# Optimization experiments

Hardware: AMD Instinct MI355X
Metric: run time of the kernel (lower is better)

## Reference

```python
import jax, jax.numpy as jnp
import numpy as np

N_POINTS = 16384  # matches init_kwargs n_points


def setup_inputs() -> dict:
    key = jax.random.key(0)
    k1, k2 = jax.random.split(key)
    B, N = 32, 524288
    p = jax.random.normal(k1, (B, N, 3), dtype=jnp.float32)
    zero_mask = jax.random.bernoulli(k2, 0.3, (B, N))
    p = jnp.where(zero_mask[..., None], 0.0, p)
    return {"pred_cloud": p}


def _sample_one(key, p):
    # p: (N, 3). Torch: non_zeros = sum(p, dim=2).ne(0); filter, then
    # randperm[:n] if enough points else randint with replacement.
    N = p.shape[0]
    mask = jnp.sum(p, axis=1) != 0              # (N,) valid points
    k = jnp.sum(mask).astype(jnp.int32)          # number of valid points
    # stable argsort puts valid (False for ~mask) indices first -> compacted index list
    order = jnp.argsort(~mask, stable=True)      # (N,)
    kperm, krep = jax.random.split(key)
    # branch A (k >= n_points): random subset without replacement among valid
    scores = jnp.where(mask, jax.random.uniform(kperm, (N,)), jnp.inf)
    perm_idx = jnp.argsort(scores)[:N_POINTS]    # (n_points,) valid indices, random order
    # branch B (k < n_points): randint(0, k) with replacement over compacted valid ids
    u = jax.random.uniform(krep, (N_POINTS,))
    rep = jnp.floor(u * k.astype(u.dtype)).astype(jnp.int32) % jnp.maximum(k, 1)
    repl_idx = order[rep]
    idx = jnp.where(k < N_POINTS, repl_idx, perm_idx)  # (n_points,)
    return p[idx]                                 # (n_points, 3)


def reference(pred_cloud):
    B = pred_cloud.shape[0]
    keys = jax.random.split(jax.random.key(42), B)
    return jax.vmap(_sample_one)(keys, pred_cloud)  # (B, n_points, 3)
```

## Files before the change

### kernel.cpp

```cpp
#include <hip/hip_runtime.h>
#include <stdint.h>

#define NB 32
#define NN 524288
#define NPTS 16384
#define NSEG 8
#define SEGCAP 4096
#define SCAP 20480
#define NBINS 4096
#define THRESH 0.0478515625f
#define CNTSTRIDE 32

struct Keys { uint32_t k[2 * NB]; };

__host__ __device__ static inline void tf2x32(uint32_t k0, uint32_t k1,
                                              uint32_t x0, uint32_t x1,
                                              uint32_t* o0, uint32_t* o1) {
  uint32_t ks2 = k0 ^ k1 ^ 0x1BD11BDAu;
  x0 += k0; x1 += k1;
#define TFR(r) { x0 += x1; x1 = (x1 << (r)) | (x1 >> (32 - (r))); x1 ^= x0; }
  TFR(13) TFR(15) TFR(26) TFR(6)
  x0 += k1; x1 += ks2 + 1u;
  TFR(17) TFR(29) TFR(16) TFR(24)
  x0 += ks2; x1 += k0 + 2u;
  TFR(13) TFR(15) TFR(26) TFR(6)
  x0 += k0; x1 += k1 + 3u;
  TFR(17) TFR(29) TFR(16) TFR(24)
  x0 += k1; x1 += ks2 + 4u;
  TFR(13) TFR(15) TFR(26) TFR(6)
  x0 += ks2; x1 += k0 + 5u;
#undef TFR
  *o0 = x0; *o1 = x1;
}

__global__ __launch_bounds__(256) void k_candidates(
    const float* __restrict__ p, Keys keys,
    uint64_t* __restrict__ cand, uint32_t* __restrict__ cand_cnt) {
  const int b = blockIdx.y;
  const int t = threadIdx.x;
  const int i0 = (blockIdx.x * 256 + t) * 4;
  const uint32_t kp0 = keys.k[2 * b], kp1 = keys.k[2 * b + 1];
  const float* pb = p + (size_t)b * NN * 3;

  uint64_t mykeys[4];
  int nc = 0;
#pragma unroll
  for (int j = 0; j < 4; ++j) {
    uint32_t o0, o1;
    tf2x32(kp0, kp1, 0u, (uint32_t)(i0 + j), &o0, &o1);
    uint32_t bits = o0 ^ o1;
    float u = __uint_as_float((bits >> 9) | 0x3F800000u) - 1.0f;
    if (u < THRESH) {
      const float* pp = pb + 3 * (size_t)(i0 + j);
      float x = pp[0], y = pp[1], z = pp[2];
      if (((x + y) + z) != 0.0f)
        mykeys[nc++] = ((uint64_t)__float_as_uint(u) << 32) | (uint32_t)(i0 + j);
    }
  }

  __shared__ uint32_t lcnt, lbase;
  if (t == 0) lcnt = 0u;
  __syncthreads();
  uint32_t loc = 0u;
  if (nc) loc = atomicAdd(&lcnt, (uint32_t)nc);
  __syncthreads();
  const int seg = blockIdx.x & (NSEG - 1);
  if (t == 0)
    lbase = atomicAdd(&cand_cnt[(b * NSEG + seg) * CNTSTRIDE], lcnt);
  __syncthreads();
  uint64_t* cb = cand + ((size_t)b * NSEG + seg) * SEGCAP;
  for (int j = 0; j < nc; ++j) {
    uint32_t slot = lbase + loc + j;
    if (slot < SEGCAP) cb[slot] = mykeys[j];
  }
}

__global__ __launch_bounds__(1024) void k_scan_scatter(
    const uint64_t* __restrict__ cand, const uint32_t* __restrict__ cand_cnt,
    uint32_t* __restrict__ cum, uint32_t* __restrict__ scount,
    uint64_t* __restrict__ sorted) {
  const int b = blockIdx.x;
  const int t = threadIdx.x;
  const int lane = t & 63, wave = t >> 6;
  __shared__ uint32_t lhist[NBINS];
  __shared__ uint32_t lcum[NBINS + 1];
  __shared__ uint32_t wsum[16];
  __shared__ uint32_t segM[NSEG];

  for (int i = t; i < NBINS; i += 1024) lhist[i] = 0u;
  if (t < NSEG) {
    uint32_t M = cand_cnt[(b * NSEG + t) * CNTSTRIDE];
    segM[t] = (M > SEGCAP) ? SEGCAP : M;
  }
  __syncthreads();

#pragma unroll
  for (int s = 0; s < NSEG; ++s) {
    const uint32_t M = segM[s];
    const uint64_t* cb = cand + ((size_t)b * NSEG + s) * SEGCAP;
    for (uint32_t j = t; j < M; j += 1024) {
      uint32_t ub = (uint32_t)(cb[j] >> 32);
      int bin = (int)(__uint_as_float(ub) * 65536.0f);
      atomicAdd(&lhist[bin], 1u);
    }
  }
  __syncthreads();

  uint32_t h0 = lhist[4 * t], h1 = lhist[4 * t + 1],
           h2 = lhist[4 * t + 2], h3 = lhist[4 * t + 3];
  uint32_t s4 = h0 + h1 + h2 + h3;
  uint32_t v = s4;
  for (int off = 1; off < 64; off <<= 1) {
    uint32_t n = __shfl_up(v, off, 64);
    if (lane >= off) v += n;
  }
  if (lane == 63) wsum[wave] = v;
  __syncthreads();
  if (t < 16) {
    uint32_t w = wsum[t];
    for (int off = 1; off < 16; off <<= 1) {
      uint32_t n = __shfl_up(w, off, 64);
      if (t >= off) w += n;
    }
    wsum[t] = w;
  }
  __syncthreads();
  uint32_t incl = v + (wave ? wsum[wave - 1] : 0u);
  uint32_t c[5];
  c[0] = incl - s4; c[1] = c[0] + h0; c[2] = c[1] + h1;
  c[3] = c[2] + h2; c[4] = incl;
  lcum[4 * t] = c[0]; lcum[4 * t + 1] = c[1];
  lcum[4 * t + 2] = c[2]; lcum[4 * t + 3] = c[3];
  if (t == 1023) lcum[NBINS] = incl;
  uint32_t* gc = cum + (size_t)b * (NBINS + 1);
  gc[4 * t] = c[0]; gc[4 * t + 1] = c[1];
  gc[4 * t + 2] = c[2]; gc[4 * t + 3] = c[3];
  if (t == 1023) gc[NBINS] = incl;
#pragma unroll
  for (int q = 0; q < 4; ++q)
    if (c[q] < NPTS && c[q + 1] >= NPTS) {
      uint32_t sc = c[q + 1];
      scount[b] = (sc > SCAP) ? SCAP : sc;
    }
  if (t == 1023 && incl < NPTS) scount[b] = incl;
  __syncthreads();

  for (int i = t; i < NBINS; i += 1024) lhist[i] = 0u;
  __syncthreads();
#pragma unroll
  for (int s = 0; s < NSEG; ++s) {
    const uint32_t M = segM[s];
    const uint64_t* cb = cand + ((size_t)b * NSEG + s) * SEGCAP;
    for (uint32_t j = t; j < M; j += 1024) {
      uint64_t key = cb[j];
      int bin = (int)(__uint_as_float((uint32_t)(key >> 32)) * 65536.0f);
      uint32_t c0 = lcum[bin];
      if (c0 < NPTS) {
        uint32_t pos = atomicAdd(&lhist[bin], 1u);
        uint32_t sl = c0 + pos;
        if (sl < SCAP) sorted[(size_t)b * SCAP + sl] = key;
      }
    }
  }
}

__global__ __launch_bounds__(256) void k_rank(
    const float* __restrict__ p, const uint64_t* __restrict__ sorted,
    const uint32_t* __restrict__ cum, const uint32_t* __restrict__ scount,
    float* __restrict__ out) {
  const int b = blockIdx.y;
  const uint32_t j = blockIdx.x * 256 + threadIdx.x;
  if (j >= scount[b]) return;
  const uint64_t* sb = sorted + (size_t)b * SCAP;
  uint64_t key = sb[j];
  float u = __uint_as_float((uint32_t)(key >> 32));
  int bin = (int)(u * 65536.0f);
  const uint32_t* gc = cum + (size_t)b * (NBINS + 1);
  uint32_t c0 = gc[bin], c1 = gc[bin + 1];
  uint32_t r = c0;
  for (uint32_t l = c0; l < c1; ++l) r += (sb[l] < key) ? 1u : 0u;
  if (r < NPTS) {
    uint32_t idx = (uint32_t)key;
    const float* pp = p + (size_t)b * NN * 3 + 3 * (size_t)idx;
    float* o = out + ((size_t)b * NPTS + r) * 3;
    o[0] = pp[0]; o[1] = pp[1]; o[2] = pp[2];
  }
}

extern "C" void kernel_launch(void* const* d_in, const int* in_sizes, int n_in,
                              void* d_out, int out_size, void* d_ws, size_t ws_size,
                              hipStream_t stream) {
  const float* p = (const float*)d_in[0];
  float* out = (float*)d_out;
  uint8_t* ws = (uint8_t*)d_ws;

  size_t off_cand   = 0;
  size_t off_sorted = off_cand + (size_t)NB * NSEG * SEGCAP * 8;
  size_t off_cum    = off_sorted + (size_t)NB * SCAP * 8;
  size_t off_scnt   = off_cum + (size_t)NB * (NBINS + 1) * 4;
  size_t off_cnt    = off_scnt + 128;
  size_t zero_bytes = (size_t)NB * NSEG * CNTSTRIDE * 4;

  uint64_t* cand     = (uint64_t*)(ws + off_cand);
  uint64_t* sorted   = (uint64_t*)(ws + off_sorted);
  uint32_t* cum      = (uint32_t*)(ws + off_cum);
  uint32_t* scount   = (uint32_t*)(ws + off_scnt);
  uint32_t* cand_cnt = (uint32_t*)(ws + off_cnt);

  Keys keys;
  for (int b = 0; b < NB; ++b) {
    uint32_t kb0, kb1, kp0, kp1;
    tf2x32(0u, 42u, 0u, (uint32_t)b, &kb0, &kb1);
    tf2x32(kb0, kb1, 0u, 0u, &kp0, &kp1);
    keys.k[2 * b] = kp0; keys.k[2 * b + 1] = kp1;
  }

  hipMemsetAsync(ws + off_cnt, 0, zero_bytes, stream);
  dim3 g1(NN / 1024, NB);
  k_candidates<<<g1, 256, 0, stream>>>(p, keys, cand, cand_cnt);
  k_scan_scatter<<<NB, 1024, 0, stream>>>(cand, cand_cnt, cum, scount, sorted);
  dim3 g4(SCAP / 256, NB);
  k_rank<<<g4, 256, 0, stream>>>(p, sorted, cum, scount, out);
}
```

Measured before the change: 308.5 us.

## Store candidates in fixed per-block slots instead of global atomic segments

Each candidate block now writes its filtered keys into a private fixed-capacity slot (BCAP entries) and records its count. This removes the global atomic append counters and the memset that zeroed them. The scan kernel maps two threads to each producer block's slot and reads per-block counts. A 2-float vector load for the point xy and removal of one barrier are also included. Any block producing more than BCAP candidates silently drops the excess. BCAP is sized for the roughly 49 expected candidates per block.

```diff
diff --git a/kernel.cpp b/kernel.cpp
--- a/kernel.cpp
+++ b/kernel.cpp
@@ -4,12 +4,11 @@
 #define NB 32
 #define NN 524288
 #define NPTS 16384
-#define NSEG 8
-#define SEGCAP 4096
+#define NBLK (NN / 1024)
+#define BCAP 96
 #define SCAP 20480
 #define NBINS 4096
 #define THRESH 0.0478515625f
-#define CNTSTRIDE 32
 
 struct Keys { uint32_t k[2 * NB]; };
 
@@ -35,12 +34,14 @@
 
 __global__ __launch_bounds__(256) void k_candidates(
     const float* __restrict__ p, Keys keys,
-    uint64_t* __restrict__ cand, uint32_t* __restrict__ cand_cnt) {
+    uint64_t* __restrict__ cand, uint32_t* __restrict__ blkcnt) {
   const int b = blockIdx.y;
+  const int bx = blockIdx.x;
   const int t = threadIdx.x;
-  const int i0 = (blockIdx.x * 256 + t) * 4;
+  const int i0 = (bx * 256 + t) * 4;
   const uint32_t kp0 = keys.k[2 * b], kp1 = keys.k[2 * b + 1];
   const float* pb = p + (size_t)b * NN * 3;
+  typedef float f2 __attribute__((ext_vector_type(2), aligned(4)));
 
   uint64_t mykeys[4];
   int nc = 0;
@@ -52,31 +53,29 @@
     float u = __uint_as_float((bits >> 9) | 0x3F800000u) - 1.0f;
     if (u < THRESH) {
       const float* pp = pb + 3 * (size_t)(i0 + j);
-      float x = pp[0], y = pp[1], z = pp[2];
-      if (((x + y) + z) != 0.0f)
+      f2 v = *(const f2*)pp;
+      float z = pp[2];
+      if (((v.x + v.y) + z) != 0.0f)
         mykeys[nc++] = ((uint64_t)__float_as_uint(u) << 32) | (uint32_t)(i0 + j);
     }
   }
 
-  __shared__ uint32_t lcnt, lbase;
+  __shared__ uint32_t lcnt;
   if (t == 0) lcnt = 0u;
   __syncthreads();
   uint32_t loc = 0u;
   if (nc) loc = atomicAdd(&lcnt, (uint32_t)nc);
   __syncthreads();
-  const int seg = blockIdx.x & (NSEG - 1);
-  if (t == 0)
-    lbase = atomicAdd(&cand_cnt[(b * NSEG + seg) * CNTSTRIDE], lcnt);
-  __syncthreads();
-  uint64_t* cb = cand + ((size_t)b * NSEG + seg) * SEGCAP;
+  uint64_t* cb = cand + ((size_t)b * NBLK + bx) * BCAP;
   for (int j = 0; j < nc; ++j) {
-    uint32_t slot = lbase + loc + j;
-    if (slot < SEGCAP) cb[slot] = mykeys[j];
-  }
+    uint32_t sl = loc + j;
+    if (sl < BCAP) cb[sl] = mykeys[j];
+  }
+  if (t == 0) blkcnt[b * NBLK + bx] = (lcnt > BCAP) ? BCAP : lcnt;
 }
 
 __global__ __launch_bounds__(1024) void k_scan_scatter(
-    const uint64_t* __restrict__ cand, const uint32_t* __restrict__ cand_cnt,
+    const uint64_t* __restrict__ cand, const uint32_t* __restrict__ blkcnt,
     uint32_t* __restrict__ cum, uint32_t* __restrict__ scount,
     uint64_t* __restrict__ sorted) {
   const int b = blockIdx.x;
@@ -85,23 +84,22 @@
   __shared__ uint32_t lhist[NBINS];
   __shared__ uint32_t lcum[NBINS + 1];
   __shared__ uint32_t wsum[16];
-  __shared__ uint32_t segM[NSEG];
+  __shared__ uint32_t lc[NBLK];
 
   for (int i = t; i < NBINS; i += 1024) lhist[i] = 0u;
-  if (t < NSEG) {
-    uint32_t M = cand_cnt[(b * NSEG + t) * CNTSTRIDE];
-    segM[t] = (M > SEGCAP) ? SEGCAP : M;
-  }
-  __syncthreads();
-
-#pragma unroll
-  for (int s = 0; s < NSEG; ++s) {
-    const uint32_t M = segM[s];
-    const uint64_t* cb = cand + ((size_t)b * NSEG + s) * SEGCAP;
-    for (uint32_t j = t; j < M; j += 1024) {
+  if (t < NBLK) {
+    uint32_t M = blkcnt[b * NBLK + t];
+    lc[t] = (M > BCAP) ? BCAP : M;
+  }
+  __syncthreads();
+
+  {
+    const int r = t >> 1;
+    const uint32_t M = lc[r];
+    const uint64_t* cb = cand + ((size_t)b * NBLK + r) * BCAP;
+    for (uint32_t j = (uint32_t)(t & 1); j < M; j += 2) {
       uint32_t ub = (uint32_t)(cb[j] >> 32);
-      int bin = (int)(__uint_as_float(ub) * 65536.0f);
-      atomicAdd(&lhist[bin], 1u);
+      atomicAdd(&lhist[(int)(__uint_as_float(ub) * 65536.0f)], 1u);
     }
   }
   __syncthreads();
@@ -143,15 +141,14 @@
       scount[b] = (sc > SCAP) ? SCAP : sc;
     }
   if (t == 1023 && incl < NPTS) scount[b] = incl;
-  __syncthreads();
 
   for (int i = t; i < NBINS; i += 1024) lhist[i] = 0u;
   __syncthreads();
-#pragma unroll
-  for (int s = 0; s < NSEG; ++s) {
-    const uint32_t M = segM[s];
-    const uint64_t* cb = cand + ((size_t)b * NSEG + s) * SEGCAP;
-    for (uint32_t j = t; j < M; j += 1024) {
+  {
+    const int r = t >> 1;
+    const uint32_t M = lc[r];
+    const uint64_t* cb = cand + ((size_t)b * NBLK + r) * BCAP;
+    for (uint32_t j = (uint32_t)(t & 1); j < M; j += 2) {
       uint64_t key = cb[j];
       int bin = (int)(__uint_as_float((uint32_t)(key >> 32)) * 65536.0f);
       uint32_t c0 = lcum[bin];
@@ -195,17 +192,16 @@
   uint8_t* ws = (uint8_t*)d_ws;
 
   size_t off_cand   = 0;
-  size_t off_sorted = off_cand + (size_t)NB * NSEG * SEGCAP * 8;
+  size_t off_sorted = off_cand + (size_t)NB * NBLK * BCAP * 8;
   size_t off_cum    = off_sorted + (size_t)NB * SCAP * 8;
   size_t off_scnt   = off_cum + (size_t)NB * (NBINS + 1) * 4;
-  size_t off_cnt    = off_scnt + 128;
-  size_t zero_bytes = (size_t)NB * NSEG * CNTSTRIDE * 4;
-
-  uint64_t* cand     = (uint64_t*)(ws + off_cand);
-  uint64_t* sorted   = (uint64_t*)(ws + off_sorted);
-  uint32_t* cum      = (uint32_t*)(ws + off_cum);
-  uint32_t* scount   = (uint32_t*)(ws + off_scnt);
-  uint32_t* cand_cnt = (uint32_t*)(ws + off_cnt);
+  size_t off_bcnt   = off_scnt + 128;
+
+  uint64_t* cand   = (uint64_t*)(ws + off_cand);
+  uint64_t* sorted = (uint64_t*)(ws + off_sorted);
+  uint32_t* cum    = (uint32_t*)(ws + off_cum);
+  uint32_t* scount = (uint32_t*)(ws + off_scnt);
+  uint32_t* blkcnt = (uint32_t*)(ws + off_bcnt);
 
   Keys keys;
   for (int b = 0; b < NB; ++b) {
@@ -215,10 +211,9 @@
     keys.k[2 * b] = kp0; keys.k[2 * b + 1] = kp1;
   }
 
-  hipMemsetAsync(ws + off_cnt, 0, zero_bytes, stream);
-  dim3 g1(NN / 1024, NB);
-  k_candidates<<<g1, 256, 0, stream>>>(p, keys, cand, cand_cnt);
-  k_scan_scatter<<<NB, 1024, 0, stream>>>(cand, cand_cnt, cum, scount, sorted);
+  dim3 g1(NBLK, NB);
+  k_candidates<<<g1, 256, 0, stream>>>(p, keys, cand, blkcnt);
+  k_scan_scatter<<<NB, 1024, 0, stream>>>(cand, blkcnt, cum, scount, sorted);
   dim3 g4(SCAP / 256, NB);
   k_rank<<<g4, 256, 0, stream>>>(p, sorted, cum, scount, out);
 }
```

After: 311.6 us, median of 2. Within noise of the previous version (+1.0%).
